# Kernel tuning notes

Measured on AMD Instinct MI355X. Metric: run time of the kernel, lower is better.

## Reference

```python
import jax, jax.numpy as jnp
import numpy as np

EXPANSION_K = 5
N_CENTERS = 8192
DIM = 512
BATCH = 4096


def setup_inputs() -> dict:
    key = jax.random.key(0)
    k1, k2, k3 = jax.random.split(key, 3)
    z = jax.random.normal(k1, (BATCH, DIM), dtype=jnp.float32)
    # learned PMField parameters: center positions and gravitational masses
    centers = jax.random.normal(k2, (N_CENTERS, DIM), dtype=jnp.float32)
    mus = jax.random.uniform(k3, (N_CENTERS,), dtype=jnp.float32, minval=0.1, maxval=1.0)
    return {"z": z, "centers": centers, "mus": mus}


def reference(z, centers, mus):
    # --- compute_center_attractions ---
    # torch.cdist(z, centers) -> Euclidean distances (B, N), computed GEMM-style
    sq = (
        jnp.sum(z * z, axis=-1, keepdims=True)          # (B, 1)
        + jnp.sum(centers * centers, axis=-1)[None, :]   # (1, N)
        - 2.0 * (z @ centers.T)                          # (B, N)
    )
    dists = jnp.sqrt(jnp.maximum(sq, 0.0))
    attractions = mus[None, :] / (dists ** 2 + 1e-6)     # (B, N)

    # --- expand_query ---
    top_vals, top_idx = jax.lax.top_k(attractions, EXPANSION_K)  # (B, k)
    weights = jax.nn.softmax(top_vals, axis=1)                    # (B, k)
    expanded_centers = centers[top_idx]                           # gather -> (B, k, D)
    comb = jnp.einsum("bkd,bk->bd", expanded_centers, weights)   # weighted center combine
    expanded_z = 0.7 * z + 0.3 * comb                             # (B, D)
    return expanded_z, attractions
```

## Files before the change

kernel.cpp:

```cpp
#include <hip/hip_runtime.h>
#include <math.h>

#define BATCH 4096
#define NC    8192
#define DIM   512
#define KEXP  5
#define NCAND 10

using bf16x8 = __attribute__((ext_vector_type(8))) short;
using f32x4  = __attribute__((ext_vector_type(4))) float;
typedef unsigned long long u64;

__device__ unsigned short g_zbf[BATCH * DIM];
__device__ unsigned short g_cbf[NC * DIM];
__device__ float g_z2[BATCH];
__device__ float g_c2[NC];

__device__ __forceinline__ unsigned short rtne_bf16(float f) {
  unsigned u = __float_as_uint(f);
  u += 0x7FFFu + ((u >> 16) & 1u);
  return (unsigned short)(u >> 16);
}

__device__ __forceinline__ void gload16(const void* g, void* l) {
  __builtin_amdgcn_global_load_lds(
      (const __attribute__((address_space(1))) void*)g,
      (__attribute__((address_space(3))) void*)l, 16, 0, 0);
}

__global__ __launch_bounds__(256) void convert_kernel(const float* __restrict__ z,
                                                      const float* __restrict__ c) {
  const size_t i = ((size_t)blockIdx.x * 256 + threadIdx.x) * 8;
  const size_t zn = (size_t)BATCH * DIM;
  const float* src;
  unsigned short* dst;
  size_t off;
  if (i < zn) { src = z; dst = g_zbf; off = i; }
  else        { src = c; dst = g_cbf; off = i - zn; }
  float4 a = *(const float4*)(src + off);
  float4 b = *(const float4*)(src + off + 4);
  uint4 o;
  o.x = (unsigned)rtne_bf16(a.x) | ((unsigned)rtne_bf16(a.y) << 16);
  o.y = (unsigned)rtne_bf16(a.z) | ((unsigned)rtne_bf16(a.w) << 16);
  o.z = (unsigned)rtne_bf16(b.x) | ((unsigned)rtne_bf16(b.y) << 16);
  o.w = (unsigned)rtne_bf16(b.z) | ((unsigned)rtne_bf16(b.w) << 16);
  *(uint4*)(dst + off) = o;
}

__global__ __launch_bounds__(128) void norms_kernel(const float* __restrict__ z,
                                                    const float* __restrict__ c) {
  int row = blockIdx.x;
  const float* src;
  float* dst;
  if (row < BATCH) { src = z + (size_t)row * DIM; dst = g_z2 + row; }
  else             { src = c + (size_t)(row - BATCH) * DIM; dst = g_c2 + (row - BATCH); }
  int t = threadIdx.x;
  float4 v = ((const float4*)src)[t];
  double acc = (double)v.x * v.x + (double)v.y * v.y + (double)v.z * v.z + (double)v.w * v.w;
#pragma unroll
  for (int off = 32; off > 0; off >>= 1) acc += __shfl_down(acc, off);
  __shared__ double wsum[2];
  if ((t & 63) == 0) wsum[t >> 6] = acc;
  __syncthreads();
  if (t == 0) *dst = (float)(wsum[0] + wsum[1]);
}

#define BM  128
#define BN  128

__global__ __launch_bounds__(256) void attr_bf16(const float* __restrict__ mus,
                                                 float* __restrict__ att) {
  __shared__ __align__(16) unsigned short Ab[2][BM * 32];
  __shared__ __align__(16) unsigned short Bb[2][BM * 32];

  const int tid  = threadIdx.x;
  const int lane = tid & 63;
  const int wv   = tid >> 6;
  const int wm   = wv >> 1;
  const int wn   = wv & 1;

  const int flat = blockIdx.x;
  const int xcd  = flat & 7;
  const int t    = flat >> 3;
  const int row0 = (xcd * 4 + (t & 3)) * BM;
  const int col0 = (t >> 2) * BN;

  const unsigned short* Ag = g_zbf + (size_t)row0 * DIM;
  const unsigned short* Bg = g_cbf + (size_t)col0 * DIM;

  const int srow = wv * 16 + (lane >> 2);
  const int sg   = (lane & 3) ^ ((lane >> 3) & 3);

  const int q  = lane >> 4;
  const int gq = q ^ (((lane & 15) >> 1) & 3);
  const int l15 = lane & 15;

  f32x4 acc[4][4] = {};

#define STAGE(S, B)                                                         \
  {                                                                         \
    const int k0_ = (S) * 32;                                               \
    _Pragma("unroll")                                                       \
    for (int inst = 0; inst < 2; ++inst) {                                  \
      const int r_ = inst * 64 + srow;                                      \
      gload16(Ag + (size_t)r_ * DIM + k0_ + sg * 8,                         \
              &Ab[B][(inst * 64 + wv * 16) * 32]);                          \
      gload16(Bg + (size_t)r_ * DIM + k0_ + sg * 8,                         \
              &Bb[B][(inst * 64 + wv * 16) * 32]);                          \
    }                                                                       \
  }

  STAGE(0, 0);
  __syncthreads();

  for (int s = 0; s < 16; ++s) {
    const int cur = s & 1;
    if (s < 15) STAGE(s + 1, cur ^ 1);

    bf16x8 fa[4], fb[4];
#pragma unroll
    for (int i = 0; i < 4; ++i) {
      const int r = wm * 64 + i * 16 + l15;
      fa[i] = *(const bf16x8*)((const char*)&Ab[cur][0] + r * 64 + gq * 16);
    }
#pragma unroll
    for (int j = 0; j < 4; ++j) {
      const int r = wn * 64 + j * 16 + l15;
      fb[j] = *(const bf16x8*)((const char*)&Bb[cur][0] + r * 64 + gq * 16);
    }
#pragma unroll
    for (int j = 0; j < 4; ++j)
#pragma unroll
      for (int i = 0; i < 4; ++i)
        acc[j][i] = __builtin_amdgcn_mfma_f32_16x16x32_bf16(fb[j], fa[i], acc[j][i], 0, 0, 0);
    __syncthreads();
  }

#pragma unroll
  for (int i = 0; i < 4; ++i) {
    const int ar = row0 + wm * 64 + i * 16 + l15;
    const float zz = g_z2[ar];
    float* dst = att + (size_t)ar * NC;
#pragma unroll
    for (int j = 0; j < 4; ++j) {
      const int gc0 = col0 + wn * 64 + j * 16 + q * 4;
      const float4 cc = *(const float4*)&g_c2[gc0];
      const float4 mu = *(const float4*)&mus[gc0];
      const float ccv[4] = {cc.x, cc.y, cc.z, cc.w};
      const float muv[4] = {mu.x, mu.y, mu.z, mu.w};
      float o[4];
#pragma unroll
      for (int r = 0; r < 4; ++r) {
        float tt  = __fadd_rn(zz, ccv[r]);
        float sq  = __fsub_rn(tt, __fmul_rn(2.0f, acc[j][i][r]));
        float d   = sqrtf(fmaxf(sq, 0.0f));
        float den = __fadd_rn(__fmul_rn(d, d), 1e-6f);
        o[r] = __fdiv_rn(muv[r], den);
      }
      *(float4*)(dst + gc0) = *(const float4*)o;
    }
  }
#undef STAGE
}

__global__ __launch_bounds__(256, 4) void topk_kernel(const float* __restrict__ att,
                                                      const float* __restrict__ z,
                                                      const float* __restrict__ centers,
                                                      const float* __restrict__ mus,
                                                      float* __restrict__ out) {
  __shared__ int selLds[4][16];
  const int lane = threadIdx.x & 63;
  const int wv   = threadIdx.x >> 6;
  const int row  = blockIdx.x * 4 + wv;
  const float4* arow4 = (const float4*)(att + (size_t)row * NC);

  u64 k[8][4];
#pragma unroll
  for (int c = 0; c < 8; ++c) {
#pragma unroll
    for (int j = 0; j < 4; ++j) k[c][j] = 0ull;
#pragma unroll
    for (int qq = 0; qq < 4; ++qq) {
      float4 v4 = arow4[c * 256 + qq * 64 + lane];
      const unsigned ib = (unsigned)(c * 1024 + qq * 256 + lane * 4);
      const float vv[4] = {v4.x, v4.y, v4.z, v4.w};
#pragma unroll
      for (int e = 0; e < 4; ++e) {
        u64 nk = ((u64)__float_as_uint(vv[e]) << 32) | (u64)(0xFFFFFFFFu - (ib + e));
        bool g0 = nk > k[c][0], g1 = nk > k[c][1], g2 = nk > k[c][2], g3 = nk > k[c][3];
        u64 t0 = k[c][0], t1 = k[c][1], t2 = k[c][2];
        k[c][0] = g0 ? nk : k[c][0];
        k[c][1] = g0 ? t0 : (g1 ? nk : k[c][1]);
        k[c][2] = g1 ? t1 : (g2 ? nk : k[c][2]);
        k[c][3] = g2 ? t2 : (g3 ? nk : k[c][3]);
      }
    }
  }

  for (int it = 0; it < NCAND; ++it) {
    u64 b = k[0][0];
#pragma unroll
    for (int c = 1; c < 8; ++c) b = (k[c][0] > b) ? k[c][0] : b;
#pragma unroll
    for (int off = 32; off > 0; off >>= 1) {
      u64 o = __shfl_xor(b, off);
      b = (o > b) ? o : b;
    }
    if (lane == 0) selLds[wv][it] = (int)(0xFFFFFFFFu - (unsigned)(b & 0xFFFFFFFFu));
#pragma unroll
    for (int c = 0; c < 8; ++c) {
      bool hit = (k[c][0] == b);
      k[c][0] = hit ? k[c][1] : k[c][0];
      k[c][1] = hit ? k[c][2] : k[c][1];
      k[c][2] = hit ? k[c][3] : k[c][2];
      k[c][3] = hit ? 0ull    : k[c][3];
    }
  }

  const float* zrow = z + (size_t)row * DIM;
  const int d0 = lane * 8;
  const float4 za = *(const float4*)(zrow + d0);
  const float4 zb = *(const float4*)(zrow + d0 + 4);
  const float myz2 = g_z2[row];

  double p[NCAND];
  int cidx[NCAND];
#pragma unroll
  for (int c = 0; c < NCAND; ++c) {
    cidx[c] = selLds[wv][c];
    const float* cp = centers + (size_t)cidx[c] * DIM + d0;
    float4 ca = *(const float4*)(cp);
    float4 cb = *(const float4*)(cp + 4);
    p[c] = (double)za.x * ca.x + (double)za.y * ca.y +
           (double)za.z * ca.z + (double)za.w * ca.w +
           (double)zb.x * cb.x + (double)zb.y * cb.y +
           (double)zb.z * cb.z + (double)zb.w * cb.w;
  }
#pragma unroll
  for (int off = 32; off > 0; off >>= 1) {
#pragma unroll
    for (int c = 0; c < NCAND; ++c) p[c] += __shfl_xor(p[c], off);
  }

  float exv[NCAND];
#pragma unroll
  for (int c = 0; c < NCAND; ++c) {
    const int ci = cidx[c];
    float dotf = (float)p[c];
    float t   = __fadd_rn(myz2, g_c2[ci]);
    float sq  = __fsub_rn(t, __fmul_rn(2.0f, dotf));
    float d   = sqrtf(fmaxf(sq, 0.0f));
    float den = __fadd_rn(__fmul_rn(d, d), 1e-6f);
    exv[c] = __fdiv_rn(mus[ci], den);
  }

  unsigned used = 0;
  float tv[KEXP]; int tix[KEXP];
#pragma unroll
  for (int s = 0; s < KEXP; ++s) {
    float bv = -INFINITY; int bi = 0x7FFFFFFF; int bc = 0;
#pragma unroll
    for (int c = 0; c < NCAND; ++c) {
      bool ok = (used & (1u << c)) == 0;
      if (ok && (exv[c] > bv || (exv[c] == bv && cidx[c] < bi))) {
        bv = exv[c]; bi = cidx[c]; bc = c;
      }
    }
    used |= (1u << bc);
    tv[s] = bv; tix[s] = bi;
  }

  float m = tv[0];
  float w[KEXP];
  float s = 0.0f;
#pragma unroll
  for (int kk = 0; kk < KEXP; ++kk) { w[kk] = expf(tv[kk] - m); s += w[kk]; }
#pragma unroll
  for (int kk = 0; kk < KEXP; ++kk) w[kk] /= s;

  float comb[8] = {0, 0, 0, 0, 0, 0, 0, 0};
#pragma unroll
  for (int kk = 0; kk < KEXP; ++kk) {
    const float* cp = centers + (size_t)tix[kk] * DIM + d0;
    float4 a = *(const float4*)(cp);
    float4 bq = *(const float4*)(cp + 4);
    comb[0] += w[kk] * a.x;  comb[1] += w[kk] * a.y;
    comb[2] += w[kk] * a.z;  comb[3] += w[kk] * a.w;
    comb[4] += w[kk] * bq.x; comb[5] += w[kk] * bq.y;
    comb[6] += w[kk] * bq.z; comb[7] += w[kk] * bq.w;
  }
  const float zv[8] = {za.x, za.y, za.z, za.w, zb.x, zb.y, zb.z, zb.w};
  float o[8];
#pragma unroll
  for (int e = 0; e < 8; ++e)
    o[e] = __fadd_rn(__fmul_rn(0.7f, zv[e]), __fmul_rn(0.3f, comb[e]));
  *(float4*)(out + (size_t)row * DIM + d0)     = *(float4*)&o[0];
  *(float4*)(out + (size_t)row * DIM + d0 + 4) = *(float4*)&o[4];
}

extern "C" void kernel_launch(void* const* d_in, const int* in_sizes, int n_in,
                              void* d_out, int out_size, void* d_ws, size_t ws_size,
                              hipStream_t stream) {
  const float* z       = (const float*)d_in[0];
  const float* centers = (const float*)d_in[1];
  const float* mus     = (const float*)d_in[2];
  float* out      = (float*)d_out;
  float* expanded = out;
  float* att      = out + (size_t)BATCH * DIM;

  convert_kernel<<<(BATCH + NC) * DIM / (256 * 8), 256, 0, stream>>>(z, centers);
  norms_kernel<<<BATCH + NC, 128, 0, stream>>>(z, centers);
  attr_bf16<<<(BATCH / BM) * (NC / BN), 256, 0, stream>>>(mus, att);
  topk_kernel<<<BATCH / 4, 256, 0, stream>>>(att, z, centers, mus, expanded);
}
```

Before: 178.2 us.

## Load GEMM MFMA fragments directly from global memory into registers, dropping LDS staging

The bf16 GEMM in the attraction kernel no longer stages A/B tiles through double-buffered LDS with global_load_lds and barriers. Each wave now loads its MFMA operand fragments straight from global memory into registers, using register double-buffering across K steps. This removes the LDS traffic and the __syncthreads calls. In exchange, waves sharing a block fetch the same rows redundantly through the cache, and register pressure goes up.

Result: slower. 225.2 us (+26.3%).

```diff
diff --git a/kernel.cpp b/kernel.cpp
--- a/kernel.cpp
+++ b/kernel.cpp
@@ -20,12 +20,6 @@
   unsigned u = __float_as_uint(f);
   u += 0x7FFFu + ((u >> 16) & 1u);
   return (unsigned short)(u >> 16);
-}
-
-__device__ __forceinline__ void gload16(const void* g, void* l) {
-  __builtin_amdgcn_global_load_lds(
-      (const __attribute__((address_space(1))) void*)g,
-      (__attribute__((address_space(3))) void*)l, 16, 0, 0);
 }
 
 __global__ __launch_bounds__(256) void convert_kernel(const float* __restrict__ z,
@@ -70,14 +64,13 @@
 
 __global__ __launch_bounds__(256) void attr_bf16(const float* __restrict__ mus,
                                                  float* __restrict__ att) {
-  __shared__ __align__(16) unsigned short Ab[2][BM * 32];
-  __shared__ __align__(16) unsigned short Bb[2][BM * 32];
-
   const int tid  = threadIdx.x;
   const int lane = tid & 63;
   const int wv   = tid >> 6;
   const int wm   = wv >> 1;
   const int wn   = wv & 1;
+  const int l15  = lane & 15;
+  const int q    = lane >> 4;
 
   const int flat = blockIdx.x;
   const int xcd  = flat & 7;
@@ -85,56 +78,42 @@
   const int row0 = (xcd * 4 + (t & 3)) * BM;
   const int col0 = (t >> 2) * BN;
 
-  const unsigned short* Ag = g_zbf + (size_t)row0 * DIM;
-  const unsigned short* Bg = g_cbf + (size_t)col0 * DIM;
-
-  const int srow = wv * 16 + (lane >> 2);
-  const int sg   = (lane & 3) ^ ((lane >> 3) & 3);
-
-  const int q  = lane >> 4;
-  const int gq = q ^ (((lane & 15) >> 1) & 3);
-  const int l15 = lane & 15;
+  const unsigned short* Abase = g_zbf + (size_t)(row0 + wm * 64 + l15) * DIM + q * 8;
+  const unsigned short* Bbase = g_cbf + (size_t)(col0 + wn * 64 + l15) * DIM + q * 8;
 
   f32x4 acc[4][4] = {};
 
-#define STAGE(S, B)                                                         \
+  bf16x8 fa0[4], fb0[4], fa1[4], fb1[4];
+
+#define LOADF(FA, FB, S)                                                    \
   {                                                                         \
-    const int k0_ = (S) * 32;                                               \
     _Pragma("unroll")                                                       \
-    for (int inst = 0; inst < 2; ++inst) {                                  \
-      const int r_ = inst * 64 + srow;                                      \
-      gload16(Ag + (size_t)r_ * DIM + k0_ + sg * 8,                         \
-              &Ab[B][(inst * 64 + wv * 16) * 32]);                          \
-      gload16(Bg + (size_t)r_ * DIM + k0_ + sg * 8,                         \
-              &Bb[B][(inst * 64 + wv * 16) * 32]);                          \
+    for (int i = 0; i < 4; ++i) {                                           \
+      FA[i] = *(const bf16x8*)(Abase + (size_t)i * 16 * DIM + (S) * 32);    \
+      FB[i] = *(const bf16x8*)(Bbase + (size_t)i * 16 * DIM + (S) * 32);    \
     }                                                                       \
   }
 
-  STAGE(0, 0);
-  __syncthreads();
-
-  for (int s = 0; s < 16; ++s) {
-    const int cur = s & 1;
-    if (s < 15) STAGE(s + 1, cur ^ 1);
-
-    bf16x8 fa[4], fb[4];
-#pragma unroll
-    for (int i = 0; i < 4; ++i) {
-      const int r = wm * 64 + i * 16 + l15;
-      fa[i] = *(const bf16x8*)((const char*)&Ab[cur][0] + r * 64 + gq * 16);
-    }
-#pragma unroll
-    for (int j = 0; j < 4; ++j) {
-      const int r = wn * 64 + j * 16 + l15;
-      fb[j] = *(const bf16x8*)((const char*)&Bb[cur][0] + r * 64 + gq * 16);
-    }
-#pragma unroll
-    for (int j = 0; j < 4; ++j)
-#pragma unroll
-      for (int i = 0; i < 4; ++i)
-        acc[j][i] = __builtin_amdgcn_mfma_f32_16x16x32_bf16(fb[j], fa[i], acc[j][i], 0, 0, 0);
-    __syncthreads();
-  }
+#define MFMAS(FA, FB)                                                       \
+  {                                                                         \
+    _Pragma("unroll")                                                       \
+    for (int j = 0; j < 4; ++j)                                             \
+      _Pragma("unroll")                                                     \
+      for (int i = 0; i < 4; ++i)                                           \
+        acc[j][i] = __builtin_amdgcn_mfma_f32_16x16x32_bf16(FB[j], FA[i],   \
+                                                            acc[j][i], 0, 0, 0); \
+  }
+
+  LOADF(fa0, fb0, 0);
+#pragma unroll
+  for (int s = 0; s < 16; s += 2) {
+    LOADF(fa1, fb1, s + 1);
+    MFMAS(fa0, fb0);
+    if (s + 2 < 16) LOADF(fa0, fb0, s + 2);
+    MFMAS(fa1, fb1);
+  }
+#undef LOADF
+#undef MFMAS
 
 #pragma unroll
   for (int i = 0; i < 4; ++i) {
@@ -160,7 +139,6 @@
       *(float4*)(dst + gc0) = *(const float4*)o;
     }
   }
-#undef STAGE
 }
 
 __global__ __launch_bounds__(256, 4) void topk_kernel(const float* __restrict__ att,
```
